# Optimization experiments

Measured on AMD Instinct MI355X. Metric: run time of the kernel, lower is better.

The kernel has to match this reference:

```python
import jax, jax.numpy as jnp
import numpy as np

HEAD_NUM = 4
B, S, D = 8, 1024, 512


def setup_inputs() -> dict:
    k = jax.random.key(0)
    kq, kk, kv = jax.random.split(k, 3)
    return {
        "query": jax.random.normal(kq, (B, S, D), dtype=jnp.float32),
        "key": jax.random.normal(kk, (B, S, D), dtype=jnp.float32),
        "value": jax.random.normal(kv, (B, S, D), dtype=jnp.float32),
    }


def _corr_attention(q, k, v):
    # q,k,v: [B, H, S, hd]
    score = jnp.einsum('bhqd,bhkd->bhqk', q, k)  # raw dot products
    len_q = jnp.sqrt(jnp.sum(q * q, axis=-1))    # [B,H,S]
    len_k = jnp.sqrt(jnp.sum(k * k, axis=-1))    # [B,H,S]
    score = score / (len_q[..., :, None] * len_k[..., None, :])  # cosine similarity
    signal = jnp.sign(score)
    flat = jnp.abs(score).reshape(-1)            # global flatten across B,H,S,S
    n = flat.shape[0]
    idx = jnp.argsort(-flat)                     # descending sort indices
    prob = (jnp.arange(n, dtype=flat.dtype) + 1.0) / n  # (1/n, 2/n, ..., 1)
    ranked = flat.at[idx].set(prob)              # rank-transform: largest -> smallest prob
    score = (-jnp.log(ranked)).reshape(signal.shape) * signal
    return jnp.einsum('bhqk,bhkd->bhqd', score, v)


def reference(query, key, value):
    b, s, d = query.shape
    h = HEAD_NUM
    q = query.reshape(b, s, h, -1).transpose(0, 2, 1, 3)
    k = key.reshape(b, s, h, -1).transpose(0, 2, 1, 3)
    v = value.reshape(b, s, h, -1).transpose(0, 2, 1, 3)
    out = _corr_attention(q, k, v)               # [B,H,S,hd]
    return out.transpose(0, 2, 1, 3).reshape(b, s, d)
```

## Files before the change

kernel.cpp:

```cpp
#include <hip/hip_runtime.h>
#include <math.h>

#define BB 8
#define SS 1024
#define DD 512
#define HH 4
#define HD 128
#define N_SC (BB*HH*SS*SS)

#define NB 8192
#define BINS 13107.2f
#define NBLK 2048
#define NP2 32

#define OFF_S     0
#define SZ_S      ((size_t)N_SC*2)
#define OFF_QN    (OFF_S + SZ_S)
#define SZ_QN     ((size_t)BB*SS*DD*2)
#define OFF_KN    (OFF_QN + SZ_QN)
#define OFF_VT    (OFF_KN + SZ_QN)
#define OFF_PARTS (OFF_VT + SZ_QN)
#define SZ_PARTS  ((size_t)NBLK*(NB/4)*4)
#define OFF_WMAG  (OFF_PARTS + SZ_PARTS)
#define OFF_PART2 (OFF_WMAG + (size_t)NB*2)

typedef __bf16 bf16x8 __attribute__((ext_vector_type(8)));
typedef float  f32x4  __attribute__((ext_vector_type(4)));
typedef unsigned short ushort_t;

__device__ __forceinline__ unsigned bf16rne(float x) {
  unsigned b = __float_as_uint(x);
  return (b + 0x7FFFu + ((b >> 16) & 1u)) >> 16;
}
__device__ __forceinline__ unsigned sbin(float s) {
  return (unsigned)fminf(fabsf(s)*BINS, 8191.0f);
}

__global__ __launch_bounds__(256) void prep_vt_kernel(
    const float* __restrict__ q, const float* __restrict__ k,
    const float* __restrict__ v,
    unsigned* __restrict__ qn, unsigned* __restrict__ kn,
    unsigned* __restrict__ vt) {
  __shared__ float T[64][65];
  int t = threadIdx.x;
  if (blockIdx.x < 16384) {
    int lane = t & 63;
    int row = blockIdx.x*4 + (t >> 6);
    const float* src; unsigned* dst; int r;
    if (row < 32768) { src = q; dst = qn; r = row; }
    else             { src = k; dst = kn; r = row - 32768; }
    int b = r >> 12, s = (r >> 2) & 1023, h = r & 3;
    float2 vv = *(const float2*)(src + ((size_t)(b*1024 + s))*512 + h*128 + lane*2);
    float sum = vv.x*vv.x + vv.y*vv.y;
    #pragma unroll
    for (int off = 32; off; off >>= 1) sum += __shfl_xor(sum, off, 64);
    float inv = rsqrtf(sum);
    unsigned u = bf16rne(vv.x*inv) | (bf16rne(vv.y*inv) << 16);
    dst[(size_t)((b*4 + h)*1024 + s)*64 + lane] = u;
  } else {
    int vb = blockIdx.x - 16384;
    int s0 = (vb & 15)*64, d0 = ((vb >> 4) & 1)*64, bh = vb >> 5;
    int b = bh >> 2, h = bh & 3;
    #pragma unroll
    for (int i = 0; i < 16; i++) {
      int idx = t + i*256, rs = idx >> 6, cd = idx & 63;
      T[rs][cd] = v[((size_t)(b*1024 + s0 + rs))*512 + h*128 + d0 + cd];
    }
    __syncthreads();
    #pragma unroll
    for (int i = 0; i < 8; i++) {
      int idx = t + i*256, rd = idx >> 5, c2 = (idx & 31)*2;
      unsigned u = bf16rne(T[c2][rd]) | (bf16rne(T[c2+1][rd]) << 16);
      vt[(size_t)(bh*128 + d0 + rd)*512 + (s0 + c2)/2] = u;
    }
  }
}

__global__ __launch_bounds__(256) void scores_hist_kernel(
    const ushort_t* __restrict__ qn, const ushort_t* __restrict__ kn,
    ushort_t* __restrict__ S, unsigned* __restrict__ parts) {
  __shared__ ushort_t Qs[128*128];
  __shared__ ushort_t Ks[128*128];
  __shared__ unsigned h8[NB/4];
  int t = threadIdx.x;
  int L = blockIdx.x;
  int bh = L & 31, tile = L >> 5;
  int sq0 = (tile >> 3)*128, sk0 = (tile & 7)*128;

  #pragma unroll
  for (int i = 0; i < 8; i++) h8[t + i*256] = 0;

  const uint4* qg = (const uint4*)qn + (size_t)(bh*1024 + sq0)*16;
  const uint4* kg = (const uint4*)kn + (size_t)(bh*1024 + sk0)*16;
  #pragma unroll
  for (int i = 0; i < 8; i++) {
    int idx = t + i*256, row = idx >> 4, g = idx & 15;
    int sw = g ^ (row & 15);
    *(uint4*)&Qs[row*128 + sw*8] = qg[row*16 + g];
    *(uint4*)&Ks[row*128 + sw*8] = kg[row*16 + g];
  }
  __syncthreads();

  int w = t >> 6, lane = t & 63, m16 = lane & 15, q2 = lane >> 4;
  int wm = (w >> 1)*64, wn = (w & 1)*64;
  f32x4 acc[4][4];
  #pragma unroll
  for (int i = 0; i < 4; i++)
    #pragma unroll
    for (int j = 0; j < 4; j++) acc[i][j] = (f32x4){0.f,0.f,0.f,0.f};

  #pragma unroll
  for (int ks = 0; ks < 4; ks++) {
    int sw = ((ks*4 + q2) ^ m16)*8;
    bf16x8 a[4], bb[4];
    #pragma unroll
    for (int i = 0; i < 4; i++) a[i]  = *(const bf16x8*)&Qs[(wm + i*16 + m16)*128 + sw];
    #pragma unroll
    for (int j = 0; j < 4; j++) bb[j] = *(const bf16x8*)&Ks[(wn + j*16 + m16)*128 + sw];
    #pragma unroll
    for (int i = 0; i < 4; i++)
      #pragma unroll
      for (int j = 0; j < 4; j++)
        acc[i][j] = __builtin_amdgcn_mfma_f32_16x16x32_bf16(a[i], bb[j], acc[i][j], 0, 0, 0);
  }

  size_t Sbase = (size_t)bh << 20;
  #pragma unroll
  for (int i = 0; i < 4; i++)
    #pragma unroll
    for (int p = 0; p < 4; p++) {
      int row = sq0 + wm + i*16 + q2*4 + p;
      #pragma unroll
      for (int j = 0; j < 4; j++) {
        int col = sk0 + wn + j*16 + m16;
        unsigned u = bf16rne(acc[i][j][p]);
        S[Sbase + ((size_t)row << 10) + col] = (ushort_t)u;
        unsigned bin = sbin(__uint_as_float(u << 16));
        atomicAdd(&h8[bin >> 2], 1u << ((bin & 3)*8));
      }
    }
  __syncthreads();

  unsigned* dst = parts + (size_t)L*(NB/4);
  #pragma unroll
  for (int i = 0; i < 8; i++) dst[t + i*256] = h8[t + i*256];
}

__global__ __launch_bounds__(256) void reduce1_kernel(
    const unsigned* __restrict__ parts, unsigned* __restrict__ parts2) {
  int g = blockIdx.x*256 + threadIdx.x;
  int p0 = blockIdx.y*64;
  unsigned s0 = 0, s1 = 0, s2 = 0, s3 = 0;
  #pragma unroll 8
  for (int p = p0; p < p0 + 64; p++) {
    unsigned w = parts[(size_t)p*(NB/4) + g];
    s0 += w & 0xFFu; s1 += (w >> 8) & 0xFFu;
    s2 += (w >> 16) & 0xFFu; s3 += w >> 24;
  }
  uint4 o = {s0, s1, s2, s3};
  ((uint4*)parts2)[(size_t)blockIdx.y*(NB/4) + g] = o;
}

__global__ __launch_bounds__(1024) void scan_kernel(
    const unsigned* __restrict__ parts2, ushort_t* __restrict__ wmag) {
  __shared__ unsigned d[1024];
  int t = threadIdx.x;
  unsigned loc[8] = {0,0,0,0,0,0,0,0};
  #pragma unroll 4
  for (int p = 0; p < NP2; p++) {
    uint4 a = ((const uint4*)parts2)[(size_t)p*(NB/4) + t*2];
    uint4 b2 = ((const uint4*)parts2)[(size_t)p*(NB/4) + t*2 + 1];
    loc[0] += a.x;  loc[1] += a.y;  loc[2] += a.z;  loc[3] += a.w;
    loc[4] += b2.x; loc[5] += b2.y; loc[6] += b2.z; loc[7] += b2.w;
  }
  unsigned tot = 0;
  #pragma unroll
  for (int j = 0; j < 8; j++) tot += loc[j];
  d[t] = tot; __syncthreads();
  for (int off = 1; off < 1024; off <<= 1) {
    unsigned x = (t >= off) ? d[t - off] : 0u;
    __syncthreads();
    d[t] += x;
    __syncthreads();
  }
  unsigned run = d[t] - tot;
  const float inv_n = 1.0f / (float)N_SC;
  #pragma unroll
  for (int j = 0; j < 8; j++) {
    run += loc[j];
    float rm = (float)(N_SC - run) + 0.5f*(float)(loc[j] + 1u);
    wmag[t*8 + j] = (ushort_t)bf16rne(-logf(rm * inv_n));
  }
}

__global__ __launch_bounds__(256) void out_kernel(
    const ushort_t* __restrict__ S, const ushort_t* __restrict__ wmag,
    const ushort_t* __restrict__ vt, float* __restrict__ out) {
  __shared__ ushort_t Vs[128*128];
  __shared__ ushort_t Wl[NB];
  int t = threadIdx.x;
  int L = blockIdx.x;
  int bh = L & 31, q0 = (L >> 5)*64;
  int b = bh >> 2, h = bh & 3;

  #pragma unroll
  for (int i = 0; i < 4; i++)
    ((uint4*)Wl)[t + i*256] = ((const uint4*)wmag)[t + i*256];

  int w = t >> 6, lane = t & 63, m16 = lane & 15, q2 = lane >> 4;
  int qw = q0 + w*16;
  const ushort_t* Srow = S + ((size_t)(bh*1024 + qw + m16) << 10);
  const uint4* vg = (const uint4*)vt + (size_t)bh*128*128;

  f32x4 oacc[8];
  #pragma unroll
  for (int j = 0; j < 8; j++) oacc[j] = (f32x4){0.f,0.f,0.f,0.f};

  for (int kc = 0; kc < 8; kc++) {
    #pragma unroll
    for (int i = 0; i < 8; i++) {
      int idx = t + i*256, row = idx >> 4, g = idx & 15;
      *(uint4*)&Vs[row*128 + (g ^ (row & 15))*8] = vg[row*128 + kc*16 + g];
    }
    __syncthreads();

    #pragma unroll
    for (int ks = 0; ks < 4; ks++) {
      uint4 sv = *(const uint4*)&Srow[kc*128 + ks*32 + q2*8];
      unsigned sc[4] = {sv.x, sv.y, sv.z, sv.w};
      union { bf16x8 v; unsigned u[4]; } af;
      #pragma unroll
      for (int m = 0; m < 4; m++) {
        float flo = __uint_as_float(sc[m] << 16);
        float fhi = __uint_as_float(sc[m] & 0xFFFF0000u);
        unsigned wlo = (flo == 0.f) ? 0u
                       : (unsigned)Wl[sbin(flo)] | ((flo < 0.f) ? 0x8000u : 0u);
        unsigned whi = (fhi == 0.f) ? 0u
                       : (unsigned)Wl[sbin(fhi)] | ((fhi < 0.f) ? 0x8000u : 0u);
        af.u[m] = wlo | (whi << 16);
      }
      int sw = ((ks*4 + q2) ^ m16)*8;
      #pragma unroll
      for (int j = 0; j < 8; j++) {
        bf16x8 bb = *(const bf16x8*)&Vs[(j*16 + m16)*128 + sw];
        oacc[j] = __builtin_amdgcn_mfma_f32_16x16x32_bf16(af.v, bb, oacc[j], 0, 0, 0);
      }
    }
    __syncthreads();
  }

  #pragma unroll
  for (int p = 0; p < 4; p++) {
    int qrow = qw + q2*4 + p;
    #pragma unroll
    for (int j = 0; j < 8; j++)
      out[(size_t)(b*1024 + qrow)*512 + h*128 + j*16 + m16] = oacc[j][p];
  }
}

extern "C" void kernel_launch(void* const* d_in, const int* in_sizes, int n_in,
                              void* d_out, int out_size, void* d_ws, size_t ws_size,
                              hipStream_t stream) {
  const float* q = (const float*)d_in[0];
  const float* k = (const float*)d_in[1];
  const float* v = (const float*)d_in[2];
  float* out = (float*)d_out;
  char* ws = (char*)d_ws;

  ushort_t* Sbuf  = (ushort_t*)(ws + OFF_S);
  unsigned* qn    = (unsigned*)(ws + OFF_QN);
  unsigned* kn    = (unsigned*)(ws + OFF_KN);
  unsigned* vtb   = (unsigned*)(ws + OFF_VT);
  unsigned* parts = (unsigned*)(ws + OFF_PARTS);
  ushort_t* wmag  = (ushort_t*)(ws + OFF_WMAG);
  unsigned* part2 = (unsigned*)(ws + OFF_PART2);

  hipLaunchKernelGGL(prep_vt_kernel, dim3(17408), dim3(256), 0, stream, q, k, v, qn, kn, vtb);
  hipLaunchKernelGGL(scores_hist_kernel, dim3(NBLK), dim3(256), 0, stream,
                     (const ushort_t*)qn, (const ushort_t*)kn, Sbuf, parts);
  hipLaunchKernelGGL(reduce1_kernel, dim3(8, NP2), dim3(256), 0, stream, parts, part2);
  hipLaunchKernelGGL(scan_kernel, dim3(1), dim3(1024), 0, stream, part2, wmag);
  hipLaunchKernelGGL(out_kernel, dim3(512), dim3(256), 0, stream,
                     (const ushort_t*)Sbuf, wmag, (const ushort_t*)vtb, out);
}
```

Before: 179.0 us.

## Split out_kernel key dimension across two wave groups with LDS reduction

Doubles out_kernel block size to 512 threads, where two groups of four waves each process half of the key range (kc chunks), each with its own V tile in shared memory. Partial accumulators from the second half are written to LDS and summed by the first half before the global store. This aims to raise wave count per block and parallelism, since only 512 blocks exist. In exchange it doubles shared memory for V and adds a reduction step through LDS.

After: 167.3 us. 6.5% less time.

```diff
diff --git a/kernel.cpp b/kernel.cpp
--- a/kernel.cpp
+++ b/kernel.cpp
@@ -193,10 +193,10 @@
   }
 }
 
-__global__ __launch_bounds__(256) void out_kernel(
+__global__ __launch_bounds__(512) void out_kernel(
     const ushort_t* __restrict__ S, const ushort_t* __restrict__ wmag,
     const ushort_t* __restrict__ vt, float* __restrict__ out) {
-  __shared__ ushort_t Vs[128*128];
+  __shared__ ushort_t Vs[2][128*128];
   __shared__ ushort_t Wl[NB];
   int t = threadIdx.x;
   int L = blockIdx.x;
@@ -204,11 +204,13 @@
   int b = bh >> 2, h = bh & 3;
 
   #pragma unroll
-  for (int i = 0; i < 4; i++)
-    ((uint4*)Wl)[t + i*256] = ((const uint4*)wmag)[t + i*256];
+  for (int i = 0; i < 2; i++)
+    ((uint4*)Wl)[t + i*512] = ((const uint4*)wmag)[t + i*512];
 
   int w = t >> 6, lane = t & 63, m16 = lane & 15, q2 = lane >> 4;
-  int qw = q0 + w*16;
+  int qt = w & 3, kh = w >> 2;
+  int qw = q0 + qt*16;
+  int half = t >> 8, tl = t & 255;
   const ushort_t* Srow = S + ((size_t)(bh*1024 + qw + m16) << 10);
   const uint4* vg = (const uint4*)vt + (size_t)bh*128*128;
 
@@ -216,14 +218,16 @@
   #pragma unroll
   for (int j = 0; j < 8; j++) oacc[j] = (f32x4){0.f,0.f,0.f,0.f};
 
-  for (int kc = 0; kc < 8; kc++) {
+  for (int kc4 = 0; kc4 < 4; kc4++) {
+    int kcs = half*4 + kc4;
     #pragma unroll
     for (int i = 0; i < 8; i++) {
-      int idx = t + i*256, row = idx >> 4, g = idx & 15;
-      *(uint4*)&Vs[row*128 + (g ^ (row & 15))*8] = vg[row*128 + kc*16 + g];
-    }
-    __syncthreads();
-
+      int idx = tl + i*256, row = idx >> 4, g = idx & 15;
+      *(uint4*)&Vs[half][row*128 + (g ^ (row & 15))*8] = vg[row*128 + kcs*16 + g];
+    }
+    __syncthreads();
+
+    int kc = kh*4 + kc4;
     #pragma unroll
     for (int ks = 0; ks < 4; ks++) {
       uint4 sv = *(const uint4*)&Srow[kc*128 + ks*32 + q2*8];
@@ -242,19 +246,35 @@
       int sw = ((ks*4 + q2) ^ m16)*8;
       #pragma unroll
       for (int j = 0; j < 8; j++) {
-        bf16x8 bb = *(const bf16x8*)&Vs[(j*16 + m16)*128 + sw];
+        bf16x8 bb = *(const bf16x8*)&Vs[kh][(j*16 + m16)*128 + sw];
         oacc[j] = __builtin_amdgcn_mfma_f32_16x16x32_bf16(af.v, bb, oacc[j], 0, 0, 0);
       }
     }
     __syncthreads();
   }
 
-  #pragma unroll
-  for (int p = 0; p < 4; p++) {
-    int qrow = qw + q2*4 + p;
+  float* R = (float*)Vs;
+  if (kh == 1) {
     #pragma unroll
     for (int j = 0; j < 8; j++)
-      out[(size_t)(b*1024 + qrow)*512 + h*128 + j*16 + m16] = oacc[j][p];
+      #pragma unroll
+      for (int p = 0; p < 4; p++)
+        R[qt*(16*129) + (q2*4 + p)*129 + j*16 + m16] = oacc[j][p];
+  }
+  __syncthreads();
+  if (kh == 0) {
+    #pragma unroll
+    for (int j = 0; j < 8; j++)
+      #pragma unroll
+      for (int p = 0; p < 4; p++)
+        oacc[j][p] += R[qt*(16*129) + (q2*4 + p)*129 + j*16 + m16];
+    #pragma unroll
+    for (int p = 0; p < 4; p++) {
+      int qrow = qw + q2*4 + p;
+      #pragma unroll
+      for (int j = 0; j < 8; j++)
+        out[(size_t)(b*1024 + qrow)*512 + h*128 + j*16 + m16] = oacc[j][p];
+    }
   }
 }
 
@@ -280,6 +300,6 @@
                      (const ushort_t*)qn, (const ushort_t*)kn, Sbuf, parts);
   hipLaunchKernelGGL(reduce1_kernel, dim3(8, NP2), dim3(256), 0, stream, parts, part2);
   hipLaunchKernelGGL(scan_kernel, dim3(1), dim3(1024), 0, stream, part2, wmag);
-  hipLaunchKernelGGL(out_kernel, dim3(512), dim3(256), 0, stream,
+  hipLaunchKernelGGL(out_kernel, dim3(512), dim3(512), 0, stream,
                      (const ushort_t*)Sbuf, wmag, (const ushort_t*)vtb, out);
 }
```

## Split out_kernel key dimension across waves, read V directly, reduce via LDS atomics

Applied to the files above, without the earlier changes.

The output kernel now uses 1024 blocks of 512 threads. Each block covers 32 query rows, and its 8 waves split the 1024 keys into four quarters. V fragments are read straight from global memory instead of being staged through a swizzled shared tile, which drops the per-chunk barriers. Partial results are combined with shared-memory float atomics, then written out coalesced. This raises parallelism and occupancy, at the cost of uncached, uncoalesced global V reads and atomic reduction overhead.

Measured after the change: 274.9 us. +53.6%, slower.

```diff
diff --git a/kernel.cpp b/kernel.cpp
--- a/kernel.cpp
+++ b/kernel.cpp
@@ -193,68 +193,63 @@
   }
 }
 
-__global__ __launch_bounds__(256) void out_kernel(
+__global__ __launch_bounds__(512, 6) void out_kernel(
     const ushort_t* __restrict__ S, const ushort_t* __restrict__ wmag,
     const ushort_t* __restrict__ vt, float* __restrict__ out) {
-  __shared__ ushort_t Vs[128*128];
   __shared__ ushort_t Wl[NB];
+  __shared__ float Ot[2][16][129];
   int t = threadIdx.x;
   int L = blockIdx.x;
-  int bh = L & 31, q0 = (L >> 5)*64;
+  int bh = L & 31, q0 = (L >> 5)*32;
   int b = bh >> 2, h = bh & 3;
 
   #pragma unroll
-  for (int i = 0; i < 4; i++)
-    ((uint4*)Wl)[t + i*256] = ((const uint4*)wmag)[t + i*256];
+  for (int i = 0; i < 2; i++)
+    ((uint4*)Wl)[t + i*512] = ((const uint4*)wmag)[t + i*512];
+  for (int i = t; i < 2*16*129; i += 512) ((float*)Ot)[i] = 0.f;
+  __syncthreads();
 
   int w = t >> 6, lane = t & 63, m16 = lane & 15, q2 = lane >> 4;
-  int qw = q0 + w*16;
-  const ushort_t* Srow = S + ((size_t)(bh*1024 + qw + m16) << 10);
-  const uint4* vg = (const uint4*)vt + (size_t)bh*128*128;
+  int qt = w & 1, kh = w >> 1;
+  int qw = q0 + qt*16;
+  const ushort_t* Srow = S + ((size_t)(bh*1024 + qw + m16) << 10) + kh*256;
+  const ushort_t* vrow = vt + ((size_t)bh*128 + m16)*1024 + kh*256;
 
   f32x4 oacc[8];
   #pragma unroll
   for (int j = 0; j < 8; j++) oacc[j] = (f32x4){0.f,0.f,0.f,0.f};
 
-  for (int kc = 0; kc < 8; kc++) {
-    #pragma unroll
-    for (int i = 0; i < 8; i++) {
-      int idx = t + i*256, row = idx >> 4, g = idx & 15;
-      *(uint4*)&Vs[row*128 + (g ^ (row & 15))*8] = vg[row*128 + kc*16 + g];
-    }
-    __syncthreads();
-
-    #pragma unroll
-    for (int ks = 0; ks < 4; ks++) {
-      uint4 sv = *(const uint4*)&Srow[kc*128 + ks*32 + q2*8];
-      unsigned sc[4] = {sv.x, sv.y, sv.z, sv.w};
-      union { bf16x8 v; unsigned u[4]; } af;
-      #pragma unroll
-      for (int m = 0; m < 4; m++) {
-        float flo = __uint_as_float(sc[m] << 16);
-        float fhi = __uint_as_float(sc[m] & 0xFFFF0000u);
-        unsigned wlo = (flo == 0.f) ? 0u
-                       : (unsigned)Wl[sbin(flo)] | ((flo < 0.f) ? 0x8000u : 0u);
-        unsigned whi = (fhi == 0.f) ? 0u
-                       : (unsigned)Wl[sbin(fhi)] | ((fhi < 0.f) ? 0x8000u : 0u);
-        af.u[m] = wlo | (whi << 16);
-      }
-      int sw = ((ks*4 + q2) ^ m16)*8;
-      #pragma unroll
-      for (int j = 0; j < 8; j++) {
-        bf16x8 bb = *(const bf16x8*)&Vs[(j*16 + m16)*128 + sw];
-        oacc[j] = __builtin_amdgcn_mfma_f32_16x16x32_bf16(af.v, bb, oacc[j], 0, 0, 0);
-      }
-    }
-    __syncthreads();
-  }
-
-  #pragma unroll
-  for (int p = 0; p < 4; p++) {
-    int qrow = qw + q2*4 + p;
-    #pragma unroll
-    for (int j = 0; j < 8; j++)
-      out[(size_t)(b*1024 + qrow)*512 + h*128 + j*16 + m16] = oacc[j][p];
+  for (int kq = 0; kq < 8; kq++) {
+    uint4 sv = *(const uint4*)&Srow[kq*32 + q2*8];
+    unsigned sc[4] = {sv.x, sv.y, sv.z, sv.w};
+    union { bf16x8 v; unsigned u[4]; } af;
+    #pragma unroll
+    for (int m = 0; m < 4; m++) {
+      float flo = __uint_as_float(sc[m] << 16);
+      float fhi = __uint_as_float(sc[m] & 0xFFFF0000u);
+      unsigned wlo = (flo == 0.f) ? 0u
+                     : (unsigned)Wl[sbin(flo)] | ((flo < 0.f) ? 0x8000u : 0u);
+      unsigned whi = (fhi == 0.f) ? 0u
+                     : (unsigned)Wl[sbin(fhi)] | ((fhi < 0.f) ? 0x8000u : 0u);
+      af.u[m] = wlo | (whi << 16);
+    }
+    #pragma unroll
+    for (int j = 0; j < 8; j++) {
+      bf16x8 bb = *(const bf16x8*)&vrow[(size_t)j*16*1024 + kq*32 + q2*8];
+      oacc[j] = __builtin_amdgcn_mfma_f32_16x16x32_bf16(af.v, bb, oacc[j], 0, 0, 0);
+    }
+  }
+
+  #pragma unroll
+  for (int j = 0; j < 8; j++)
+    #pragma unroll
+    for (int p = 0; p < 4; p++)
+      atomicAdd(&Ot[qt][q2*4 + p][j*16 + m16], oacc[j][p]);
+  __syncthreads();
+
+  for (int i = t; i < 2*16*128; i += 512) {
+    int qt2 = i >> 11, r = (i >> 7) & 15, c = i & 127;
+    out[((size_t)(b*1024 + q0 + qt2*16 + r))*512 + h*128 + c] = Ot[qt2][r][c];
   }
 }
 
@@ -280,6 +275,6 @@
                      (const ushort_t*)qn, (const ushort_t*)kn, Sbuf, parts);
   hipLaunchKernelGGL(reduce1_kernel, dim3(8, NP2), dim3(256), 0, stream, parts, part2);
   hipLaunchKernelGGL(scan_kernel, dim3(1), dim3(1024), 0, stream, part2, wmag);
-  hipLaunchKernelGGL(out_kernel, dim3(512), dim3(256), 0, stream,
+  hipLaunchKernelGGL(out_kernel, dim3(1024), dim3(512), 0, stream,
                      (const ushort_t*)Sbuf, wmag, (const ushort_t*)vtb, out);
 }
```
